# Optimization experiments

Hardware: AMD Instinct MI355X
Metric: run time of the kernel (lower is better)

The kernel has to match this reference:

```python
import jax, jax.numpy as jnp
import numpy as np

N, E, F, H, D, C = 50000, 800000, 128, 8, 16, 40


def setup_inputs() -> dict:
    key = jax.random.key(0)
    ks = jax.random.split(key, 12)
    s_in = 1.0 / np.sqrt(F)
    s_h = 1.0 / np.sqrt(H * D)
    return {
        "x": jax.random.normal(ks[0], (N, F), jnp.float32),
        "edge_index": jax.random.randint(ks[1], (2, E), 0, N, jnp.int64),
        "W1": jax.random.normal(ks[2], (F, H * D), jnp.float32) * s_in,
        "a_src1": jax.random.normal(ks[3], (H, D), jnp.float32) * s_h,
        "a_dst1": jax.random.normal(ks[4], (H, D), jnp.float32) * s_h,
        "b1": jnp.zeros((H * D,), jnp.float32),
        "W2": jax.random.normal(ks[5], (H * D, H * D), jnp.float32) * s_h,
        "a_src2": jax.random.normal(ks[6], (H, D), jnp.float32) * s_h,
        "a_dst2": jax.random.normal(ks[7], (H, D), jnp.float32) * s_h,
        "b2": jnp.zeros((H * D,), jnp.float32),
        "Wc": jax.random.normal(ks[8], (H * D, C), jnp.float32) * s_h,
        "bc": jnp.zeros((C,), jnp.float32),
    }


def _gat_layer(x, src, dst, W, a_src, a_dst, b):
    # x: [N, F_in]; src/dst: [E'] (self-loops already appended)
    n = x.shape[0]
    h, d = a_src.shape
    hx = (x @ W).reshape(n, h, d)                      # [N, H, D]
    al_src = jnp.einsum("nhd,hd->nh", hx, a_src)       # [N, H]
    al_dst = jnp.einsum("nhd,hd->nh", hx, a_dst)       # [N, H]
    e = jax.nn.leaky_relu(al_src[src] + al_dst[dst], 0.2)  # [E', H]
    # segment softmax over incoming edges of each destination node
    m = jax.ops.segment_max(e, dst, num_segments=n)    # [N, H]
    e = jnp.exp(e - m[dst])
    z = jax.ops.segment_sum(e, dst, num_segments=n)    # [N, H]
    alpha = e / z[dst]                                 # [E', H]
    out = jax.ops.segment_sum(alpha[:, :, None] * hx[src], dst, num_segments=n)
    return out.reshape(n, h * d) + b


def reference(x, edge_index, W1, a_src1, a_dst1, b1, W2, a_src2, a_dst2, b2, Wc, bc):
    n = x.shape[0]
    loops = jnp.arange(n, dtype=edge_index.dtype)
    src = jnp.concatenate([edge_index[0], loops])  # PyG GATConv adds self-loops
    dst = jnp.concatenate([edge_index[1], loops])
    h = _gat_layer(x, src, dst, W1, a_src1, a_dst1, b1)
    h = jax.nn.elu(h)  # ELU between layers (i < K-1); dropout=None -> no-op
    h = _gat_layer(h, src, dst, W2, a_src2, a_dst2, b2)
    return h @ Wc + bc  # [N, C] logits
```

## Files before the change

kernel.cpp:

```cpp
#include <hip/hip_runtime.h>
#include <hip/hip_bf16.h>
#include <hip/hip_fp16.h>


#define FDIM 128
#define HEADS 8

typedef short bf16x8 __attribute__((ext_vector_type(8)));
typedef float f32x4 __attribute__((ext_vector_type(4)));

__device__ __forceinline__ float leaky02(float x) {
    return fmaxf(x, 0.2f * x);
}

__device__ __forceinline__ unsigned pack2h(float x, float y) {
    __half2 h2 = __floats2half2_rn(x, y);
    return *(unsigned*)&h2;
}

__device__ __forceinline__ void split2(float x, unsigned short& hi, unsigned short& lo) {
    unsigned bits = __float_as_uint(x);
    unsigned h = bits + 0x7fffu + ((bits >> 16) & 1u);
    hi = (unsigned short)(h >> 16);
    float hf = __uint_as_float(h & 0xffff0000u);
    float r = x - hf;
    unsigned rb = __float_as_uint(r);
    unsigned l2 = rb + 0x7fffu + ((rb >> 16) & 1u);
    lo = (unsigned short)(l2 >> 16);
}


__global__ __launch_bounds__(256) void prep_kernel(const int* __restrict__ ei,
                                                   int* __restrict__ deg,
                                                   int* __restrict__ rank,
                                                   int E,
                                                   const float* __restrict__ x,
                                                   unsigned short* __restrict__ x_hi,
                                                   unsigned short* __restrict__ x_lo,
                                                   int nel,
                                                   const float* __restrict__ W1,
                                                   const float* __restrict__ W2,
                                                   unsigned short* __restrict__ w1_hi,
                                                   unsigned short* __restrict__ w1_lo,
                                                   unsigned short* __restrict__ w2_hi,
                                                   unsigned short* __restrict__ w2_lo,
                                                   int histB, int xB) {
    int b = blockIdx.x, t = threadIdx.x;
    if (b < histB) {
        int e = b * 256 + t;
        if (e < E) rank[e] = atomicAdd(&deg[ei[E + e]], 1);
        return;
    }
    b -= histB;
    if (b < xB) {
        int i0 = (b * 256 + t) * 8;
        if (i0 < nel) {
            float4 v0 = *(const float4*)&x[i0];
            float4 v1 = *(const float4*)&x[i0 + 4];
            float vv[8] = {v0.x, v0.y, v0.z, v0.w, v1.x, v1.y, v1.z, v1.w};
            unsigned short h[8], l[8];
#pragma unroll
            for (int j = 0; j < 8; ++j) split2(vv[j], h[j], l[j]);
            uint4 hh, ll;
            hh.x = h[0] | ((unsigned)h[1] << 16);
            hh.y = h[2] | ((unsigned)h[3] << 16);
            hh.z = h[4] | ((unsigned)h[5] << 16);
            hh.w = h[6] | ((unsigned)h[7] << 16);
            ll.x = l[0] | ((unsigned)l[1] << 16);
            ll.y = l[2] | ((unsigned)l[3] << 16);
            ll.z = l[4] | ((unsigned)l[5] << 16);
            ll.w = l[6] | ((unsigned)l[7] << 16);
            *(uint4*)&x_hi[i0] = hh;
            *(uint4*)&x_lo[i0] = ll;
        }
        return;
    }
    b -= xB;
    const float* W = (b < 16) ? W1 : W2;
    unsigned short* whi = (b < 16) ? w1_hi : w2_hi;
    unsigned short* wlo = (b < 16) ? w1_lo : w2_lo;
    int idx = (b & 15) * 256 + t;
    int k = idx >> 5;
    int c0 = (idx & 31) * 4;
#pragma unroll
    for (int i = 0; i < 4; ++i) {
        int c = c0 + i;
        float v = W[k * FDIM + c];
        unsigned short h, l;
        split2(v, h, l);
        int dest = ((k >> 5) * 8 + (c >> 4)) * 512 +
                   ((c & 15) + (((k >> 3) & 3) << 4)) * 8 + (k & 7);
        whi[dest] = h;
        wlo[dest] = l;
    }
}


__global__ __launch_bounds__(256) void scan_partial(const int* __restrict__ deg,
                                                    int* __restrict__ partials,
                                                    int n) {
    __shared__ int red[256];
    int t = threadIdx.x;
    int base = blockIdx.x * 1024 + t * 4;
    int s = 0;
#pragma unroll
    for (int j = 0; j < 4; ++j) {
        int i = base + j;
        if (i < n) s += deg[i];
    }
    red[t] = s;
    __syncthreads();
    for (int off = 128; off > 0; off >>= 1) {
        if (t < off) red[t] += red[t + off];
        __syncthreads();
    }
    if (t == 0) partials[blockIdx.x] = red[0];
}

__global__ __launch_bounds__(256) void scan_final(const int* __restrict__ deg,
                                                  const int* __restrict__ partials,
                                                  int* __restrict__ row_start,
                                                  int n, int nb) {
    __shared__ int sbuf[256];
    __shared__ int boff_s, total_s;
    int t = threadIdx.x;
    if (t < 64) {
        int carry = 0;
        for (int base = 0; base < nb; base += 64) {
            int idx = base + t;
            int v = (idx < nb) ? partials[idx] : 0;
            int incl = v;
#pragma unroll
            for (int off = 1; off < 64; off <<= 1) {
                int x = __shfl_up(incl, off);
                if (t >= off) incl += x;
            }
            if (idx == (int)blockIdx.x) boff_s = carry + incl - v;
            carry += __shfl(incl, 63);
        }
        if (t == 0) total_s = carry;
    }
    __syncthreads();
    if (blockIdx.x == 0 && t == 0) row_start[n] = total_s;

    int base = blockIdx.x * 1024 + t * 4;
    int v[4];
#pragma unroll
    for (int j = 0; j < 4; ++j) v[j] = (base + j < n) ? deg[base + j] : 0;
    int tsum = v[0] + v[1] + v[2] + v[3];
    sbuf[t] = tsum;
    __syncthreads();
    for (int off = 1; off < 256; off <<= 1) {
        int tmp = (t >= off) ? sbuf[t - off] : 0;
        __syncthreads();
        sbuf[t] += tmp;
        __syncthreads();
    }
    int toff = boff_s + sbuf[t] - tsum;
    int run = 0;
#pragma unroll
    for (int j = 0; j < 4; ++j) {
        int i = base + j;
        if (i < n) row_start[i] = toff + run;
        run += v[j];
    }
}


template <bool SCATTER>
__global__ __launch_bounds__(256, 4) void gemm_mfma(const unsigned short* __restrict__ a_hi,
                                                    const unsigned short* __restrict__ a_lo,
                                                    const unsigned short* __restrict__ w_hi,
                                                    const unsigned short* __restrict__ w_lo,
                                                    const float* __restrict__ asrc,
                                                    const float* __restrict__ adst,
                                                    float* __restrict__ als,
                                                    float* __restrict__ ald,
                                                    unsigned* __restrict__ hxf,
                                                    int n,
                                                    const int* __restrict__ ei,
                                                    const int* __restrict__ rank,
                                                    const int* __restrict__ row_start,
                                                    int* __restrict__ csr_src,
                                                    int E, int ng, int grid) {
    int tid = threadIdx.x;
    int gb;
    if (SCATTER) {
        int bid = blockIdx.x;
        int t0 = (int)((long long)bid * ng / grid);
        int t1 = (int)((long long)(bid + 1) * ng / grid);
        if (t1 == t0) {
            int sb = bid - t0;
#pragma unroll
            for (int j = 0; j < 4; ++j) {
                int e = sb * 1024 + j * 256 + tid;
                if (e < E) {
                    int s = ei[e];
                    int d = ei[E + e];
                    __builtin_nontemporal_store(s, &csr_src[row_start[d] + rank[e]]);
                }
            }
            return;
        }
        gb = t0;
    } else {
        gb = blockIdx.x;
    }

    int lane = tid & 63;
    int wave = tid >> 6;
    int l15 = lane & 15;
    int lg = lane >> 4;
    int row0 = gb * 32;

    f32x4 acc[2][2];
#pragma unroll
    for (int fr = 0; fr < 2; ++fr)
#pragma unroll
        for (int fc = 0; fc < 2; ++fc)
#pragma unroll
            for (int r = 0; r < 4; ++r) acc[fr][fc][r] = 0.f;

#pragma unroll
    for (int kc = 0; kc < 4; ++kc) {
        bf16x8 Ah[2], Al[2], Bh[2], Bl[2];
#pragma unroll
        for (int fr = 0; fr < 2; ++fr) {
            int r = row0 + fr * 16 + l15;
            if (r > n - 1) r = n - 1;
            size_t off = (size_t)r * FDIM + kc * 32 + lg * 8;
            Ah[fr] = *(const bf16x8*)(a_hi + off);
            Al[fr] = *(const bf16x8*)(a_lo + off);
        }
#pragma unroll
        for (int fc = 0; fc < 2; ++fc) {
            int FC = wave * 2 + fc;
            size_t off = (size_t)(kc * 8 + FC) * 512 + lane * 8;
            Bh[fc] = *(const bf16x8*)(w_hi + off);
            Bl[fc] = *(const bf16x8*)(w_lo + off);
        }
#pragma unroll
        for (int fr = 0; fr < 2; ++fr)
#pragma unroll
            for (int fc = 0; fc < 2; ++fc) {
                acc[fr][fc] = __builtin_amdgcn_mfma_f32_16x16x32_bf16(
                    Al[fr], Bh[fc], acc[fr][fc], 0, 0, 0);
                acc[fr][fc] = __builtin_amdgcn_mfma_f32_16x16x32_bf16(
                    Ah[fr], Bl[fc], acc[fr][fc], 0, 0, 0);
                acc[fr][fc] = __builtin_amdgcn_mfma_f32_16x16x32_bf16(
                    Ah[fr], Bh[fc], acc[fr][fc], 0, 0, 0);
            }
    }

#pragma unroll
    for (int fr = 0; fr < 2; ++fr)
#pragma unroll
        for (int fc = 0; fc < 2; ++fc) {
            int CB = wave * 32 + fc * 16;
            int col = CB + l15;
            float as_ = asrc[col];
            float ad_ = adst[col];
#pragma unroll
            for (int reg = 0; reg < 4; ++reg) {
                int row = row0 + fr * 16 + lg * 4 + reg;
                float v = acc[fr][fc][reg];
                float vn = __shfl_xor(v, 1);
                if ((lane & 1) == 0 && row < n)
                    hxf[(size_t)row * 64 + (col >> 1)] = pack2h(v, vn);
                float ps = v * as_;
                float pd = v * ad_;
                ps += __shfl_xor(ps, 1);
                pd += __shfl_xor(pd, 1);
                ps += __shfl_xor(ps, 2);
                pd += __shfl_xor(pd, 2);
                ps += __shfl_xor(ps, 4);
                pd += __shfl_xor(pd, 4);
                ps += __shfl_xor(ps, 8);
                pd += __shfl_xor(pd, 8);
                if (l15 == 0 && row < n) {
                    als[row * HEADS + (CB >> 4)] = ps;
                    ald[row * HEADS + (CB >> 4)] = pd;
                }
            }
        }
}


__global__ __launch_bounds__(256, 8) void gemm_cls(const unsigned* __restrict__ h_f16,
                                                   const float* __restrict__ W,
                                                   const float* __restrict__ bias,
                                                   float* __restrict__ out,
                                                   int n) {
    __shared__ float xs[32][136];
    __shared__ float ws[32][48];
    int tid = threadIdx.x;
    int row0 = blockIdx.x * 128;
    int lane = tid & 63;
    int wave = tid >> 6;
    int lane2 = lane * 2;
    int wc = wave * 10;

    float acc[2][10];
#pragma unroll
    for (int i = 0; i < 2; ++i)
#pragma unroll
        for (int j = 0; j < 10; ++j) acc[i][j] = 0.f;

    for (int kc = 0; kc < 128; kc += 32) {
        if (kc) __syncthreads();
#pragma unroll
        for (int it = 0; it < 4; ++it) {
            int idx = it * 256 + tid;
            int r = idx >> 3, kg = (idx & 7) * 4;
            float4 v = make_float4(0.f, 0.f, 0.f, 0.f);
            if (row0 + r < n) {
                uint2 hh = *(const uint2*)&h_f16[(size_t)(row0 + r) * 64 + (kc + kg) / 2];
                float2 a = __half22float2(*(__half2*)&hh.x);
                float2 b = __half22float2(*(__half2*)&hh.y);
                v.x = a.x; v.y = a.y; v.z = b.x; v.w = b.y;
            }
            int col = r ^ kg;
            xs[kg + 0][col] = v.x;
            xs[kg + 1][col] = v.y;
            xs[kg + 2][col] = v.z;
            xs[kg + 3][col] = v.w;
        }
#pragma unroll
        for (int it = 0; it < 6; ++it) {
            int idx = it * 256 + tid;
            int kk = idx / 48, c = idx - kk * 48;
            ws[kk][c] = (c < 40) ? W[(size_t)(kc + kk) * 40 + c] : 0.f;
        }
        __syncthreads();
#pragma unroll
        for (int k = 0; k < 32; ++k) {
            int s = ((k >> 2) & 7) << 2;
            float2 av2 = *(const float2*)&xs[k][lane2 ^ s];
            float av[2] = {av2.x, av2.y};
#pragma unroll
            for (int j = 0; j < 10; ++j) {
                float w = ws[k][wc + j];
                acc[0][j] += av[0] * w;
                acc[1][j] += av[1] * w;
            }
        }
    }

#pragma unroll
    for (int i = 0; i < 2; ++i) {
        int row = row0 + lane2 + i;
        if (row < n) {
#pragma unroll
            for (int j = 0; j < 10; ++j)
                out[(size_t)row * 40 + wc + j] = acc[i][j] + bias[wc + j];
        }
    }
}


template <bool DOELU, bool WRITELO>
__global__ __launch_bounds__(256) void gat_aggregate(const unsigned* __restrict__ hxf,
                                                     const float* __restrict__ als,
                                                     const float* __restrict__ ald,
                                                     const int* __restrict__ row_start,
                                                     const int* __restrict__ csr_src,
                                                     const float* __restrict__ bias,
                                                     unsigned* __restrict__ h_hi,
                                                     unsigned* __restrict__ h_lo,
                                                     int n) {
    int wid = threadIdx.x >> 6;
    int lane = threadIdx.x & 63;
    int node = blockIdx.x * 4 + wid;
    if (node >= n) return;

    int rs = row_start[node];
    int deg = row_start[node + 1] - rs;

    int h = lane & 7;
    int hc = lane >> 3;
    int lq = lane >> 3;
    float ald_h = ald[node * HEADS + h];

    float acc0 = 0.f, acc1 = 0.f, zown = 0.f;
    int total = deg + 1;

    int ii = lq;
    int srcv = (ii < deg) ? csr_src[rs + ii] : node;
    float w = (ii < total) ? __expf(leaky02(als[srcv * HEADS + h] + ald_h)) : 0.f;

    int i0 = 0;
    for (; i0 + 8 <= total; i0 += 8) {
        zown += w;
        int ii_n = i0 + 8 + lq;
        int srcv_n = (ii_n < deg) ? csr_src[rs + ii_n] : node;
#pragma unroll
        for (int e = 0; e < 8; ++e) {
            int s = __builtin_amdgcn_readlane(srcv, e * 8);
            float we = __shfl(w, e * 8 + hc);
            unsigned v = hxf[(size_t)s * 64 + lane];
            float2 f = __half22float2(*(__half2*)&v);
            acc0 += we * f.x;
            acc1 += we * f.y;
        }
        float w_n = (ii_n < total) ? __expf(leaky02(als[srcv_n * HEADS + h] + ald_h)) : 0.f;
        srcv = srcv_n;
        w = w_n;
    }
    int rem = total - i0;
    if (rem > 0) {
        zown += w;
        for (int e = 0; e < rem; ++e) {
            int s = __builtin_amdgcn_readlane(srcv, e * 8);
            float we = __shfl(w, e * 8 + hc);
            unsigned v = hxf[(size_t)s * 64 + lane];
            float2 f = __half22float2(*(__half2*)&v);
            acc0 += we * f.x;
            acc1 += we * f.y;
        }
    }

    zown += __shfl_xor(zown, 8);
    zown += __shfl_xor(zown, 16);
    zown += __shfl_xor(zown, 32);
    float z = __shfl(zown, hc);

    float2 bv = *(const float2*)&bias[2 * lane];
    float o0 = acc0 / z + bv.x;
    float o1 = acc1 / z + bv.y;
    if (DOELU) {
        o0 = o0 > 0.f ? o0 : (__expf(o0) - 1.f);
        o1 = o1 > 0.f ? o1 : (__expf(o1) - 1.f);
    }
    if (WRITELO) {
        unsigned short hh0, ll0, hh1, ll1;
        split2(o0, hh0, ll0);
        split2(o1, hh1, ll1);
        h_hi[(size_t)node * 64 + lane] = (unsigned)hh0 | ((unsigned)hh1 << 16);
        h_lo[(size_t)node * 64 + lane] = (unsigned)ll0 | ((unsigned)ll1 << 16);
    } else {
        h_hi[(size_t)node * 64 + lane] = pack2h(o0, o1);
    }
}


extern "C" void kernel_launch(void* const* d_in, const int* in_sizes, int n_in,
                              void* d_out, int out_size, void* d_ws, size_t ws_size,
                              hipStream_t stream) {
    const float* x      = (const float*)d_in[0];
    const int*   ei     = (const int*)d_in[1];
    const float* W1     = (const float*)d_in[2];
    const float* a_src1 = (const float*)d_in[3];
    const float* a_dst1 = (const float*)d_in[4];
    const float* b1     = (const float*)d_in[5];
    const float* W2     = (const float*)d_in[6];
    const float* a_src2 = (const float*)d_in[7];
    const float* a_dst2 = (const float*)d_in[8];
    const float* b2     = (const float*)d_in[9];
    const float* Wc     = (const float*)d_in[10];
    const float* bc     = (const float*)d_in[11];
    float* out = (float*)d_out;

    const int N = in_sizes[0] / FDIM;
    const int E = in_sizes[1] / 2;
    const int NB = (N + 1023) / 1024;
    const int nel = N * FDIM;

    unsigned* hxf = (unsigned*)d_ws;
    unsigned* xh_u = hxf + (size_t)N * 64;
    unsigned* xl_u = xh_u + (size_t)N * 64;
    float* als  = (float*)(xl_u + (size_t)N * 64);
    float* ald  = als + (size_t)N * HEADS;
    unsigned short* w1_hi = (unsigned short*)(ald + (size_t)N * HEADS);
    unsigned short* w1_lo = w1_hi + 16384;
    unsigned short* w2_hi = w1_lo + 16384;
    unsigned short* w2_lo = w2_hi + 16384;
    int* deg       = (int*)(w2_lo + 16384);
    int* row_start = deg + N;
    int* partials  = row_start + ((N + 8) & ~3);
    int* rank      = partials + ((NB + 4) & ~3);
    int* csr_src   = rank + E;

    unsigned short* x_hi = (unsigned short*)xh_u;
    unsigned short* x_lo = (unsigned short*)xl_u;

    hipMemsetAsync(deg, 0, (size_t)N * sizeof(int), stream);
    const int histB = (E + 255) / 256;
    const int xB = (nel + 2047) / 2048;
    prep_kernel<<<histB + xB + 32, 256, 0, stream>>>(
        ei, deg, rank, E, x, x_hi, x_lo, nel,
        W1, W2, w1_hi, w1_lo, w2_hi, w2_lo, histB, xB);
    scan_partial<<<NB, 256, 0, stream>>>(deg, partials, N);
    scan_final<<<NB, 256, 0, stream>>>(deg, partials, row_start, N, NB);

    const int ng = (N + 31) / 32;
    const int ns = (E + 1023) / 1024;
    const int grid1 = ng + ns;
    const int agg_grid = (N + 3) / 4;
    const int cls_grid = (N + 127) / 128;

    gemm_mfma<true><<<grid1, 256, 0, stream>>>(x_hi, x_lo, w1_hi, w1_lo,
                                               a_src1, a_dst1, als, ald, hxf, N,
                                               ei, rank, row_start, csr_src,
                                               E, ng, grid1);
    gat_aggregate<true, true><<<agg_grid, 256, 0, stream>>>(
        hxf, als, ald, row_start, csr_src, b1, xh_u, xl_u, N);
    gemm_mfma<false><<<ng, 256, 0, stream>>>(x_hi, x_lo, w2_hi, w2_lo,
                                             a_src2, a_dst2, als, ald, hxf, N,
                                             nullptr, nullptr, nullptr, nullptr,
                                             0, ng, ng);
    gat_aggregate<false, false><<<agg_grid, 256, 0, stream>>>(
        hxf, als, ald, row_start, csr_src, b2, xh_u, xl_u, N);
    gemm_cls<<<cls_grid, 256, 0, stream>>>(xh_u, Wc, bc, out, N);
}
```

Measured before the change: 226.6 us.

## Fuse fp32-to-bf16 split of x into layer-1 GEMM and rearrange CSR build

The x hi/lo bf16 split pass is removed. The layer-1 GEMM now reads fp32 x directly and splits it in registers, using truncation instead of rounding for the hi part. The degree histogram moves from the prep kernel into the spare blocks of the layer-1 GEMM, and the CSR scatter becomes its own kernel after the scan. This saves the write and reread of the x_hi/x_lo arrays, at the cost of one more kernel launch and slightly different rounding of the split.

```diff
diff --git a/kernel.cpp b/kernel.cpp
--- a/kernel.cpp
+++ b/kernel.cpp
@@ -30,52 +30,13 @@
 }
 
 
-__global__ __launch_bounds__(256) void prep_kernel(const int* __restrict__ ei,
-                                                   int* __restrict__ deg,
-                                                   int* __restrict__ rank,
-                                                   int E,
-                                                   const float* __restrict__ x,
-                                                   unsigned short* __restrict__ x_hi,
-                                                   unsigned short* __restrict__ x_lo,
-                                                   int nel,
-                                                   const float* __restrict__ W1,
-                                                   const float* __restrict__ W2,
-                                                   unsigned short* __restrict__ w1_hi,
-                                                   unsigned short* __restrict__ w1_lo,
-                                                   unsigned short* __restrict__ w2_hi,
-                                                   unsigned short* __restrict__ w2_lo,
-                                                   int histB, int xB) {
+__global__ __launch_bounds__(256) void wconv_kernel(const float* __restrict__ W1,
+                                                    const float* __restrict__ W2,
+                                                    unsigned short* __restrict__ w1_hi,
+                                                    unsigned short* __restrict__ w1_lo,
+                                                    unsigned short* __restrict__ w2_hi,
+                                                    unsigned short* __restrict__ w2_lo) {
     int b = blockIdx.x, t = threadIdx.x;
-    if (b < histB) {
-        int e = b * 256 + t;
-        if (e < E) rank[e] = atomicAdd(&deg[ei[E + e]], 1);
-        return;
-    }
-    b -= histB;
-    if (b < xB) {
-        int i0 = (b * 256 + t) * 8;
-        if (i0 < nel) {
-            float4 v0 = *(const float4*)&x[i0];
-            float4 v1 = *(const float4*)&x[i0 + 4];
-            float vv[8] = {v0.x, v0.y, v0.z, v0.w, v1.x, v1.y, v1.z, v1.w};
-            unsigned short h[8], l[8];
-#pragma unroll
-            for (int j = 0; j < 8; ++j) split2(vv[j], h[j], l[j]);
-            uint4 hh, ll;
-            hh.x = h[0] | ((unsigned)h[1] << 16);
-            hh.y = h[2] | ((unsigned)h[3] << 16);
-            hh.z = h[4] | ((unsigned)h[5] << 16);
-            hh.w = h[6] | ((unsigned)h[7] << 16);
-            ll.x = l[0] | ((unsigned)l[1] << 16);
-            ll.y = l[2] | ((unsigned)l[3] << 16);
-            ll.z = l[4] | ((unsigned)l[5] << 16);
-            ll.w = l[6] | ((unsigned)l[7] << 16);
-            *(uint4*)&x_hi[i0] = hh;
-            *(uint4*)&x_lo[i0] = ll;
-        }
-        return;
-    }
-    b -= xB;
     const float* W = (b < 16) ? W1 : W2;
     unsigned short* whi = (b < 16) ? w1_hi : w2_hi;
     unsigned short* wlo = (b < 16) ? w1_lo : w2_lo;
@@ -167,8 +128,27 @@
 }
 
 
-template <bool SCATTER>
-__global__ __launch_bounds__(256, 4) void gemm_mfma(const unsigned short* __restrict__ a_hi,
+__global__ __launch_bounds__(256) void scatter_kernel(const int* __restrict__ ei,
+                                                      const int* __restrict__ rank,
+                                                      const int* __restrict__ row_start,
+                                                      int* __restrict__ csr_src,
+                                                      int E) {
+    int tid = threadIdx.x;
+#pragma unroll
+    for (int j = 0; j < 4; ++j) {
+        int e = blockIdx.x * 1024 + j * 256 + tid;
+        if (e < E) {
+            int s = ei[e];
+            int d = ei[E + e];
+            __builtin_nontemporal_store(s, &csr_src[row_start[d] + rank[e]]);
+        }
+    }
+}
+
+
+template <bool FUSED>
+__global__ __launch_bounds__(256, 4) void gemm_mfma(const float* __restrict__ xf,
+                                                    const unsigned short* __restrict__ a_hi,
                                                     const unsigned short* __restrict__ a_lo,
                                                     const unsigned short* __restrict__ w_hi,
                                                     const unsigned short* __restrict__ w_lo,
@@ -179,13 +159,12 @@
                                                     unsigned* __restrict__ hxf,
                                                     int n,
                                                     const int* __restrict__ ei,
-                                                    const int* __restrict__ rank,
-                                                    const int* __restrict__ row_start,
-                                                    int* __restrict__ csr_src,
+                                                    int* __restrict__ deg,
+                                                    int* __restrict__ rank,
                                                     int E, int ng, int grid) {
     int tid = threadIdx.x;
     int gb;
-    if (SCATTER) {
+    if (FUSED) {
         int bid = blockIdx.x;
         int t0 = (int)((long long)bid * ng / grid);
         int t1 = (int)((long long)(bid + 1) * ng / grid);
@@ -194,11 +173,7 @@
 #pragma unroll
             for (int j = 0; j < 4; ++j) {
                 int e = sb * 1024 + j * 256 + tid;
-                if (e < E) {
-                    int s = ei[e];
-                    int d = ei[E + e];
-                    __builtin_nontemporal_store(s, &csr_src[row_start[d] + rank[e]]);
-                }
+                if (e < E) rank[e] = atomicAdd(&deg[ei[E + e]], 1);
             }
             return;
         }
@@ -228,9 +203,23 @@
         for (int fr = 0; fr < 2; ++fr) {
             int r = row0 + fr * 16 + l15;
             if (r > n - 1) r = n - 1;
-            size_t off = (size_t)r * FDIM + kc * 32 + lg * 8;
-            Ah[fr] = *(const bf16x8*)(a_hi + off);
-            Al[fr] = *(const bf16x8*)(a_lo + off);
+            if (FUSED) {
+                const float* px = xf + (size_t)r * FDIM + kc * 32 + lg * 8;
+                float4 v0 = *(const float4*)px;
+                float4 v1 = *(const float4*)(px + 4);
+                float vv[8] = {v0.x, v0.y, v0.z, v0.w, v1.x, v1.y, v1.z, v1.w};
+#pragma unroll
+                for (int j = 0; j < 8; ++j) {
+                    unsigned bits = __float_as_uint(vv[j]);
+                    Ah[fr][j] = (short)(bits >> 16);
+                    float hf = __uint_as_float(bits & 0xffff0000u);
+                    Al[fr][j] = (short)(__float_as_uint(vv[j] - hf) >> 16);
+                }
+            } else {
+                size_t off = (size_t)r * FDIM + kc * 32 + lg * 8;
+                Ah[fr] = *(const bf16x8*)(a_hi + off);
+                Al[fr] = *(const bf16x8*)(a_lo + off);
+            }
         }
 #pragma unroll
         for (int fc = 0; fc < 2; ++fc) {
@@ -464,6 +453,7 @@
     const int E = in_sizes[1] / 2;
     const int NB = (N + 1023) / 1024;
     const int nel = N * FDIM;
+    (void)nel;
 
     unsigned* hxf = (unsigned*)d_ws;
     unsigned* xh_u = hxf + (size_t)N * 64;
@@ -480,34 +470,31 @@
     int* rank      = partials + ((NB + 4) & ~3);
     int* csr_src   = rank + E;
 
-    unsigned short* x_hi = (unsigned short*)xh_u;
-    unsigned short* x_lo = (unsigned short*)xl_u;
-
     hipMemsetAsync(deg, 0, (size_t)N * sizeof(int), stream);
-    const int histB = (E + 255) / 256;
-    const int xB = (nel + 2047) / 2048;
-    prep_kernel<<<histB + xB + 32, 256, 0, stream>>>(
-        ei, deg, rank, E, x, x_hi, x_lo, nel,
-        W1, W2, w1_hi, w1_lo, w2_hi, w2_lo, histB, xB);
+    wconv_kernel<<<32, 256, 0, stream>>>(W1, W2, w1_hi, w1_lo, w2_hi, w2_lo);
+
+    const int ng = (N + 31) / 32;
+    const int hb = (E + 1023) / 1024;
+    const int grid1 = ng + hb;
+    const int agg_grid = (N + 3) / 4;
+    const int cls_grid = (N + 127) / 128;
+
+    gemm_mfma<true><<<grid1, 256, 0, stream>>>(x, nullptr, nullptr,
+                                               w1_hi, w1_lo,
+                                               a_src1, a_dst1, als, ald, hxf, N,
+                                               ei, deg, rank, E, ng, grid1);
     scan_partial<<<NB, 256, 0, stream>>>(deg, partials, N);
     scan_final<<<NB, 256, 0, stream>>>(deg, partials, row_start, N, NB);
-
-    const int ng = (N + 31) / 32;
-    const int ns = (E + 1023) / 1024;
-    const int grid1 = ng + ns;
-    const int agg_grid = (N + 3) / 4;
-    const int cls_grid = (N + 127) / 128;
-
-    gemm_mfma<true><<<grid1, 256, 0, stream>>>(x_hi, x_lo, w1_hi, w1_lo,
-                                               a_src1, a_dst1, als, ald, hxf, N,
-                                               ei, rank, row_start, csr_src,
-                                               E, ng, grid1);
+    scatter_kernel<<<hb, 256, 0, stream>>>(ei, rank, row_start, csr_src, E);
+
     gat_aggregate<true, true><<<agg_grid, 256, 0, stream>>>(
         hxf, als, ald, row_start, csr_src, b1, xh_u, xl_u, N);
-    gemm_mfma<false><<<ng, 256, 0, stream>>>(x_hi, x_lo, w2_hi, w2_lo,
+    gemm_mfma<false><<<ng, 256, 0, stream>>>(nullptr,
+                                             (const unsigned short*)xh_u,
+                                             (const unsigned short*)xl_u,
+                                             w2_hi, w2_lo,
                                              a_src2, a_dst2, als, ald, hxf, N,
-                                             nullptr, nullptr, nullptr, nullptr,
-                                             0, ng, ng);
+                                             nullptr, nullptr, nullptr, 0, ng, ng);
     gat_aggregate<false, false><<<agg_grid, 256, 0, stream>>>(
         hxf, als, ald, row_start, csr_src, b2, xh_u, xl_u, N);
     gemm_cls<<<cls_grid, 256, 0, stream>>>(xh_u, Wc, bc, out, N);
```

Measured after the change: 222.9 us. Within noise of the previous version (-1.6%).
